# Optimization experiments

Hardware: AMD Instinct MI355X
Metric: run time of the kernel (lower is better)

## Reference

```python
import jax, jax.numpy as jnp
import numpy as np

B, S, H = 4, 2048, 1024   # batch, seq, hidden
D = 2048                  # expert intermediate (SwiGLU MLP)
E = 8                     # n_routed_experts
K = 2                     # num_experts_per_tok


def setup_inputs() -> dict:
    key = jax.random.key(0)
    ks = jax.random.split(key, 8)
    w = lambda k, shape: (jax.random.normal(k, shape, jnp.float32) * 0.02)
    return {
        "hidden_states": jax.random.normal(ks[0], (B, S, H), jnp.float32),
        "gate_w": w(ks[1], (H, E)),       # router logits projection
        "w_gate": w(ks[2], (E, H, D)),    # routed experts: gate_proj
        "w_up":   w(ks[3], (E, H, D)),    # routed experts: up_proj
        "w_down": w(ks[4], (E, D, H)),    # routed experts: down_proj
        "ws_gate": w(ks[5], (H, D)),      # shared expert: gate_proj
        "ws_up":   w(ks[6], (H, D)),      # shared expert: up_proj
        "ws_down": w(ks[7], (D, H)),      # shared expert: down_proj
    }


def reference(hidden_states, gate_w, w_gate, w_up, w_down, ws_gate, ws_up, ws_down):
    b, s, h = hidden_states.shape
    x = hidden_states.reshape(-1, h)                      # [N, H], N = B*S

    # --- MoeGate: softmax over experts, top-k, renormalize top-k weights ---
    scores = jax.nn.softmax(x @ gate_w, axis=-1)          # [N, E]
    topk_w, topk_idx = jax.lax.top_k(scores, K)           # [N, K]
    topk_w = topk_w / (jnp.sum(topk_w, axis=-1, keepdims=True) + 1e-20)

    # Combine per-token top-k weights into a dense per-expert weight [N, E].
    # Equivalent to the sort-based dispatch + index_add combine in the original:
    # each token's output is sum_k topk_w[n,k] * expert_{topk_idx[n,k]}(x[n]).
    onehot = jax.nn.one_hot(topk_idx, E, dtype=x.dtype)   # [N, K, E]
    w_per_expert = jnp.einsum('nke,nk->ne', onehot, topk_w)  # [N, E]

    # --- routed experts (SwiGLU MLP), fixed small loop over experts ---
    y = jnp.zeros_like(x)
    for e in range(E):
        hid = jax.nn.silu(x @ w_gate[e]) * (x @ w_up[e])  # [N, D]
        y = y + w_per_expert[:, e:e + 1] * (hid @ w_down[e])

    # --- shared expert applied to all tokens ---
    shared = (jax.nn.silu(x @ ws_gate) * (x @ ws_up)) @ ws_down
    return (y + shared).reshape(b, s, h)
```

## Files before the change

kernel.cpp:

```cpp
#include <hip/hip_runtime.h>
#include <hip/hip_bf16.h>
#include <stdint.h>

#define N_TOK 8192
#define H_DIM 1024
#define D_DIM 2048
#define NEXP  8

#define NSLOT      16384
#define SHARED_ROW 16512
#define HID_ROWS   24704

typedef __attribute__((ext_vector_type(8))) short          bf16x8;
typedef __attribute__((ext_vector_type(4))) float          f32x4;
typedef __attribute__((ext_vector_type(8))) unsigned short u16x8;

__device__ __forceinline__ unsigned short f2bf(float f) {
    union { float f; uint32_t u; } v; v.f = f;
    uint32_t r = v.u + 0x7fff + ((v.u >> 16) & 1);
    return (unsigned short)(r >> 16);
}

__device__ __forceinline__ void gll16(const void* g, void* l) {
    __builtin_amdgcn_global_load_lds(
        (const __attribute__((address_space(1))) void*)g,
        (__attribute__((address_space(3))) void*)l, 16, 0, 0);
}

__global__ void k_router(const float* __restrict__ x, const float* __restrict__ gw,
                         int* __restrict__ tok_e, float* __restrict__ tok_w,
                         int* __restrict__ counts) {
    int l = threadIdx.x & 63;
    int n = blockIdx.x * 4 + (threadIdx.x >> 6);
    const float* xr = x + (size_t)n * H_DIM + l * 16;
    float acc[NEXP];
#pragma unroll
    for (int e = 0; e < NEXP; ++e) acc[e] = 0.f;
#pragma unroll
    for (int j = 0; j < 16; ++j) {
        float xv = xr[j];
        const float4* g4 = (const float4*)(gw + (size_t)(l * 16 + j) * NEXP);
        float4 g0 = g4[0], g1 = g4[1];
        acc[0] += xv * g0.x; acc[1] += xv * g0.y; acc[2] += xv * g0.z; acc[3] += xv * g0.w;
        acc[4] += xv * g1.x; acc[5] += xv * g1.y; acc[6] += xv * g1.z; acc[7] += xv * g1.w;
    }
#pragma unroll
    for (int off = 32; off >= 1; off >>= 1) {
#pragma unroll
        for (int e = 0; e < NEXP; ++e) acc[e] += __shfl_xor(acc[e], off);
    }
    if (l == 0) {
        int e0 = 0; float v0 = acc[0];
#pragma unroll
        for (int e = 1; e < NEXP; ++e) if (acc[e] > v0) { v0 = acc[e]; e0 = e; }
        int e1 = -1; float v1 = -1e30f;
#pragma unroll
        for (int e = 0; e < NEXP; ++e) if (e != e0 && acc[e] > v1) { v1 = acc[e]; e1 = e; }
        float t  = expf(v1 - v0);
        float w1 = t / (1.f + t);
        float w0 = 1.f - w1;
        tok_e[2 * n]     = e0;  tok_e[2 * n + 1] = e1;
        tok_w[2 * n]     = w0;  tok_w[2 * n + 1] = w1;
        atomicAdd(&counts[e0], 1);
        atomicAdd(&counts[e1], 1);
    }
}

__global__ void k_scan(const int* __restrict__ counts, int* __restrict__ offs) {
    if (threadIdx.x == 0) {
        int s = 0;
        for (int e = 0; e < NEXP; ++e) { offs[e] = s; s += counts[e]; }
    }
}

__global__ void k_assign(const int* __restrict__ tok_e, const float* __restrict__ tok_w,
                         const int* __restrict__ offs, int* __restrict__ cursor,
                         int* __restrict__ slot_token, float* __restrict__ slot_weight) {
    int n = blockIdx.x * 256 + threadIdx.x;
#pragma unroll
    for (int k = 0; k < 2; ++k) {
        int e   = tok_e[2 * n + k];
        float w = tok_w[2 * n + k];
        int pos = atomicAdd(&cursor[e], 1);
        int s   = offs[e] + pos;
        slot_token[s]  = n;
        slot_weight[s] = w;
    }
}

__global__ void k_cvt_x(const float* __restrict__ x, unsigned short* __restrict__ xb) {
    size_t i = ((size_t)blockIdx.x * 256 + threadIdx.x) * 8;
    float4 a = *(const float4*)(x + i);
    float4 b = *(const float4*)(x + i + 4);
    u16x8 o;
    o[0] = f2bf(a.x); o[1] = f2bf(a.y); o[2] = f2bf(a.z); o[3] = f2bf(a.w);
    o[4] = f2bf(b.x); o[5] = f2bf(b.y); o[6] = f2bf(b.z); o[7] = f2bf(b.w);
    *(u16x8*)(xb + i) = o;
}

__global__ void k_tconv(const float* __restrict__ src, unsigned short* __restrict__ dst,
                        int R, int C) {
    __shared__ float tb[64][65];
    size_t mb = (size_t)blockIdx.z * (size_t)R * C;
    src += mb; dst += mb;
    int t = threadIdx.x;
    int r0 = blockIdx.y * 64, c0 = blockIdx.x * 64;
    int c4 = t & 15, rr = t >> 4;
#pragma unroll
    for (int p = 0; p < 4; ++p) {
        int r = p * 16 + rr;
        float4 v = *(const float4*)(src + (size_t)(r0 + r) * C + c0 + c4 * 4);
        tb[r][c4 * 4 + 0] = v.x; tb[r][c4 * 4 + 1] = v.y;
        tb[r][c4 * 4 + 2] = v.z; tb[r][c4 * 4 + 3] = v.w;
    }
    __syncthreads();
    int rbase = (t & 7) * 8;
#pragma unroll
    for (int p = 0; p < 2; ++p) {
        int cc = p * 32 + (t >> 3);
        u16x8 o;
#pragma unroll
        for (int j = 0; j < 8; ++j) o[j] = f2bf(tb[rbase + j][cc]);
        *(u16x8*)(dst + (size_t)(c0 + cc) * R + r0 + rbase) = o;
    }
}

__global__ __launch_bounds__(256, 4) void k_gemm1(
    const unsigned short* __restrict__ xb,
    const unsigned short* __restrict__ wg_t, const unsigned short* __restrict__ wu_t,
    const unsigned short* __restrict__ wsg_t, const unsigned short* __restrict__ wsu_t,
    const int* __restrict__ counts, const int* __restrict__ offs,
    const int* __restrict__ slot_token, const float* __restrict__ slot_weight,
    unsigned short* __restrict__ hid) {
    int g = blockIdx.z;
    int n_g, sbase, hbase;
    if (g < NEXP) { n_g = counts[g]; sbase = offs[g]; hbase = sbase; }
    else          { n_g = N_TOK;     sbase = 0;       hbase = SHARED_ROW; }
    int rt = blockIdx.y;
    if (rt * 128 >= n_g) return;
    int dt = blockIdx.x;

    const unsigned short* Bg = (g < NEXP) ? wg_t + (size_t)g * D_DIM * H_DIM : wsg_t;
    const unsigned short* Bu = (g < NEXP) ? wu_t + (size_t)g * D_DIM * H_DIM : wsu_t;

    __shared__ __attribute__((aligned(16))) char smem[32 * 1024];
    __shared__ float sWt[128];
    char* sA  = smem;
    char* sBg = smem + 16384;
    char* sBu = smem + 24576;

    int t = threadIdx.x;
    int w = t >> 6, l = t & 63;
    if (t < 128) {
        int r = rt * 128 + t;
        sWt[t] = (g < NEXP) ? ((r < n_g) ? slot_weight[sbase + r] : 0.f) : 1.f;
    }
    int lr8 = l >> 3, lc8 = l & 7;
    int swz = ((lc8 ^ lr8) << 4);

    const char* aptr[4]; char* ldsa[4];
#pragma unroll
    for (int c = 0; c < 4; ++c) {
        int chunk = w * 4 + c;
        int row = chunk * 8 + lr8;
        int r = rt * 128 + row;
        int tk;
        if (g == NEXP) tk = r;
        else           tk = (r < n_g) ? slot_token[sbase + r] : slot_token[sbase];
        aptr[c] = (const char*)xb + ((size_t)tk * H_DIM) * 2 + swz;
        ldsa[c] = sA + chunk * 1024;
    }
    const char* bgptr[2]; const char* buptr[2]; char* ldsbg[2]; char* ldsbu[2];
#pragma unroll
    for (int c = 0; c < 2; ++c) {
        int chunk = w * 2 + c;
        int row = chunk * 8 + lr8;
        int nn = dt * 64 + row;
        bgptr[c] = (const char*)Bg + ((size_t)nn * H_DIM) * 2 + swz;
        buptr[c] = (const char*)Bu + ((size_t)nn * H_DIM) * 2 + swz;
        ldsbg[c] = sBg + chunk * 1024;
        ldsbu[c] = sBu + chunk * 1024;
    }

    f32x4 accg[4][2], accu[4][2];
#pragma unroll
    for (int m = 0; m < 4; ++m)
#pragma unroll
        for (int n = 0; n < 2; ++n) { accg[m][n] = 0.f; accu[m][n] = 0.f; }

    int wr = w >> 1, wc = w & 1;
    int lr = l & 15, lg = l >> 4;
    int rsw = (lr & 7) << 4;

    for (int ks = 0; ks < H_DIM / 64; ++ks) {
        int kb = ks * 128;
#pragma unroll
        for (int c = 0; c < 4; ++c) gll16(aptr[c] + kb, ldsa[c]);
#pragma unroll
        for (int c = 0; c < 2; ++c) {
            gll16(bgptr[c] + kb, ldsbg[c]);
            gll16(buptr[c] + kb, ldsbu[c]);
        }
        __syncthreads();
#pragma unroll
        for (int ksub = 0; ksub < 2; ++ksub) {
            int c0 = (ksub * 64 + lg * 16) ^ rsw;
            bf16x8 a[4], bg[2], bu[2];
#pragma unroll
            for (int m = 0; m < 4; ++m)
                a[m] = *(const bf16x8*)(sA + (wr * 64 + m * 16 + lr) * 128 + c0);
#pragma unroll
            for (int n = 0; n < 2; ++n) {
                bg[n] = *(const bf16x8*)(sBg + (wc * 32 + n * 16 + lr) * 128 + c0);
                bu[n] = *(const bf16x8*)(sBu + (wc * 32 + n * 16 + lr) * 128 + c0);
            }
#pragma unroll
            for (int m = 0; m < 4; ++m)
#pragma unroll
                for (int n = 0; n < 2; ++n) {
                    accg[m][n] = __builtin_amdgcn_mfma_f32_16x16x32_bf16(a[m], bg[n], accg[m][n], 0, 0, 0);
                    accu[m][n] = __builtin_amdgcn_mfma_f32_16x16x32_bf16(a[m], bu[n], accu[m][n], 0, 0, 0);
                }
        }
        __syncthreads();
    }

    int cb = dt * 64 + wc * 32;
#pragma unroll
    for (int m = 0; m < 4; ++m)
#pragma unroll
        for (int n = 0; n < 2; ++n)
#pragma unroll
            for (int i = 0; i < 4; ++i) {
                int trow = wr * 64 + m * 16 + lg * 4 + i;
                int row = rt * 128 + trow;
                if (row < n_g) {
                    float gv = accg[m][n][i], uv = accu[m][n][i];
                    float hv = (gv / (1.f + __expf(-gv))) * uv * sWt[trow];
                    int col = cb + n * 16 + lr;
                    hid[(size_t)(hbase + row) * D_DIM + col] = f2bf(hv);
                }
            }
}

template <int MODE>
__global__ __launch_bounds__(256, 4) void k_gemm2(
    const unsigned short* __restrict__ hid,
    const unsigned short* __restrict__ wd_t, const unsigned short* __restrict__ wsd_t,
    const int* __restrict__ counts, const int* __restrict__ offs,
    const int* __restrict__ slot_token, float* __restrict__ out) {
    int n_g, abase;
    const unsigned short* B;
    if (MODE == 0) { n_g = N_TOK; abase = SHARED_ROW; B = wsd_t; }
    else {
        int g = blockIdx.z;
        n_g = counts[g]; abase = offs[g];
        B = wd_t + (size_t)g * H_DIM * D_DIM;
    }
    int rt = blockIdx.y;
    if (rt * 128 >= n_g) return;
    int ct = blockIdx.x;

    __shared__ __attribute__((aligned(16))) char smem[24 * 1024];
    __shared__ int sTok[128];
    char* sA = smem;
    char* sB = smem + 16384;

    int t = threadIdx.x, w = t >> 6, l = t & 63;
    if (MODE == 1 && t < 128) {
        int r = rt * 128 + t;
        sTok[t] = (r < n_g) ? slot_token[abase + r] : 0;
    }
    int lr8 = l >> 3, lc8 = l & 7;
    int swz = ((lc8 ^ lr8) << 4);
    const char* aptr[4]; char* ldsa[4];
#pragma unroll
    for (int c = 0; c < 4; ++c) {
        int chunk = w * 4 + c;
        int row = chunk * 8 + lr8;
        aptr[c] = (const char*)hid + ((size_t)(abase + rt * 128 + row) * D_DIM) * 2 + swz;
        ldsa[c] = sA + chunk * 1024;
    }
    const char* bptr[2]; char* ldsb[2];
#pragma unroll
    for (int c = 0; c < 2; ++c) {
        int chunk = w * 2 + c;
        int row = chunk * 8 + lr8;
        bptr[c] = (const char*)B + ((size_t)(ct * 64 + row) * D_DIM) * 2 + swz;
        ldsb[c] = sB + chunk * 1024;
    }
    f32x4 acc[4][2];
#pragma unroll
    for (int m = 0; m < 4; ++m)
#pragma unroll
        for (int n = 0; n < 2; ++n) acc[m][n] = 0.f;

    int wr = w >> 1, wc = w & 1, lr = l & 15, lg = l >> 4;
    int rsw = (lr & 7) << 4;

    for (int ks = 0; ks < D_DIM / 64; ++ks) {
        int kb = ks * 128;
#pragma unroll
        for (int c = 0; c < 4; ++c) gll16(aptr[c] + kb, ldsa[c]);
#pragma unroll
        for (int c = 0; c < 2; ++c) gll16(bptr[c] + kb, ldsb[c]);
        __syncthreads();
#pragma unroll
        for (int ksub = 0; ksub < 2; ++ksub) {
            int c0 = (ksub * 64 + lg * 16) ^ rsw;
            bf16x8 a[4], b[2];
#pragma unroll
            for (int m = 0; m < 4; ++m)
                a[m] = *(const bf16x8*)(sA + (wr * 64 + m * 16 + lr) * 128 + c0);
#pragma unroll
            for (int n = 0; n < 2; ++n)
                b[n] = *(const bf16x8*)(sB + (wc * 32 + n * 16 + lr) * 128 + c0);
#pragma unroll
            for (int m = 0; m < 4; ++m)
#pragma unroll
                for (int n = 0; n < 2; ++n)
                    acc[m][n] = __builtin_amdgcn_mfma_f32_16x16x32_bf16(a[m], b[n], acc[m][n], 0, 0, 0);
        }
        __syncthreads();
    }

    int cb = ct * 64 + wc * 32;
#pragma unroll
    for (int m = 0; m < 4; ++m)
#pragma unroll
        for (int n = 0; n < 2; ++n)
#pragma unroll
            for (int i = 0; i < 4; ++i) {
                int tr = wr * 64 + m * 16 + lg * 4 + i;
                int col = cb + n * 16 + lr;
                if (MODE == 0) {
                    out[(size_t)(rt * 128 + tr) * H_DIM + col] = acc[m][n][i];
                } else {
                    if (rt * 128 + tr < n_g) {
                        int tok = sTok[tr];
                        unsafeAtomicAdd(&out[(size_t)tok * H_DIM + col], acc[m][n][i]);
                    }
                }
            }
}

extern "C" void kernel_launch(void* const* d_in, const int* in_sizes, int n_in,
                              void* d_out, int out_size, void* d_ws, size_t ws_size,
                              hipStream_t stream) {
    const float* x       = (const float*)d_in[0];
    const float* gw      = (const float*)d_in[1];
    const float* w_gate  = (const float*)d_in[2];
    const float* w_up    = (const float*)d_in[3];
    const float* w_down  = (const float*)d_in[4];
    const float* ws_gate = (const float*)d_in[5];
    const float* ws_up   = (const float*)d_in[6];
    const float* ws_down = (const float*)d_in[7];
    float* out = (float*)d_out;
    char* ws = (char*)d_ws;

    const size_t oXB    = 0;
    const size_t oWG    = oXB    + (size_t)N_TOK * H_DIM * 2;
    const size_t oWU    = oWG    + (size_t)NEXP * D_DIM * H_DIM * 2;
    const size_t oWD    = oWU    + (size_t)NEXP * D_DIM * H_DIM * 2;
    const size_t oWSG   = oWD    + (size_t)NEXP * H_DIM * D_DIM * 2;
    const size_t oWSU   = oWSG   + (size_t)D_DIM * H_DIM * 2;
    const size_t oWSD   = oWSU   + (size_t)D_DIM * H_DIM * 2;
    const size_t oHID   = oWSD   + (size_t)H_DIM * D_DIM * 2;
    const size_t oTOKE  = oHID   + (size_t)HID_ROWS * D_DIM * 2;
    const size_t oTOKW  = oTOKE  + (size_t)N_TOK * 2 * 4;
    const size_t oSLOTT = oTOKW  + (size_t)N_TOK * 2 * 4;
    const size_t oSLOTW = oSLOTT + (size_t)(NSLOT + 128) * 4;
    const size_t oCTRL  = oSLOTW + (size_t)(NSLOT + 128) * 4;

    unsigned short* xb    = (unsigned short*)(ws + oXB);
    unsigned short* wg_t  = (unsigned short*)(ws + oWG);
    unsigned short* wu_t  = (unsigned short*)(ws + oWU);
    unsigned short* wd_t  = (unsigned short*)(ws + oWD);
    unsigned short* wsg_t = (unsigned short*)(ws + oWSG);
    unsigned short* wsu_t = (unsigned short*)(ws + oWSU);
    unsigned short* wsd_t = (unsigned short*)(ws + oWSD);
    unsigned short* hid   = (unsigned short*)(ws + oHID);
    int*   tok_e       = (int*)(ws + oTOKE);
    float* tok_w       = (float*)(ws + oTOKW);
    int*   slot_token  = (int*)(ws + oSLOTT);
    float* slot_weight = (float*)(ws + oSLOTW);
    int*   counts      = (int*)(ws + oCTRL);
    int*   offs        = counts + 8;
    int*   cursor      = counts + 16;

    hipMemsetAsync(counts, 0, 256, stream);
    k_router<<<N_TOK / 4, 256, 0, stream>>>(x, gw, tok_e, tok_w, counts);
    k_scan<<<1, 64, 0, stream>>>(counts, offs);
    k_assign<<<N_TOK / 256, 256, 0, stream>>>(tok_e, tok_w, offs, cursor, slot_token, slot_weight);

    k_cvt_x<<<(N_TOK * H_DIM) / (8 * 256), 256, 0, stream>>>(x, xb);
    k_tconv<<<dim3(D_DIM / 64, H_DIM / 64, NEXP), 256, 0, stream>>>(w_gate, wg_t, H_DIM, D_DIM);
    k_tconv<<<dim3(D_DIM / 64, H_DIM / 64, NEXP), 256, 0, stream>>>(w_up,   wu_t, H_DIM, D_DIM);
    k_tconv<<<dim3(H_DIM / 64, D_DIM / 64, NEXP), 256, 0, stream>>>(w_down, wd_t, D_DIM, H_DIM);
    k_tconv<<<dim3(D_DIM / 64, H_DIM / 64, 1),    256, 0, stream>>>(ws_gate, wsg_t, H_DIM, D_DIM);
    k_tconv<<<dim3(D_DIM / 64, H_DIM / 64, 1),    256, 0, stream>>>(ws_up,   wsu_t, H_DIM, D_DIM);
    k_tconv<<<dim3(H_DIM / 64, D_DIM / 64, 1),    256, 0, stream>>>(ws_down, wsd_t, D_DIM, H_DIM);

    k_gemm1<<<dim3(32, 64, NEXP + 1), 256, 0, stream>>>(xb, wg_t, wu_t, wsg_t, wsu_t,
                                                        counts, offs, slot_token, slot_weight, hid);
    k_gemm2<0><<<dim3(16, 64, 1), 256, 0, stream>>>(hid, wd_t, wsd_t, counts, offs,
                                                    slot_token, out);
    k_gemm2<1><<<dim3(16, 64, NEXP), 256, 0, stream>>>(hid, wd_t, wsd_t, counts, offs,
                                                       slot_token, out);
}
```

Measured before the change: 936.4 us.

## Fuse routing/dispatch, merge weight conversions, replace atomic combine with slot buffer

```diff
diff --git a/kernel.cpp b/kernel.cpp
--- a/kernel.cpp
+++ b/kernel.cpp
@@ -29,82 +29,112 @@
 
 __global__ void k_router(const float* __restrict__ x, const float* __restrict__ gw,
                          int* __restrict__ tok_e, float* __restrict__ tok_w,
-                         int* __restrict__ counts) {
+                         unsigned short* __restrict__ xb) {
     int l = threadIdx.x & 63;
     int n = blockIdx.x * 4 + (threadIdx.x >> 6);
-    const float* xr = x + (size_t)n * H_DIM + l * 16;
+    const float4* xr4 = (const float4*)(x + (size_t)n * H_DIM + l * 16);
+    float4 v0 = xr4[0], v1 = xr4[1], v2 = xr4[2], v3 = xr4[3];
+    float xv[16] = {v0.x, v0.y, v0.z, v0.w, v1.x, v1.y, v1.z, v1.w,
+                    v2.x, v2.y, v2.z, v2.w, v3.x, v3.y, v3.z, v3.w};
     float acc[NEXP];
 #pragma unroll
     for (int e = 0; e < NEXP; ++e) acc[e] = 0.f;
 #pragma unroll
     for (int j = 0; j < 16; ++j) {
-        float xv = xr[j];
+        float xvj = xv[j];
         const float4* g4 = (const float4*)(gw + (size_t)(l * 16 + j) * NEXP);
         float4 g0 = g4[0], g1 = g4[1];
-        acc[0] += xv * g0.x; acc[1] += xv * g0.y; acc[2] += xv * g0.z; acc[3] += xv * g0.w;
-        acc[4] += xv * g1.x; acc[5] += xv * g1.y; acc[6] += xv * g1.z; acc[7] += xv * g1.w;
-    }
+        acc[0] += xvj * g0.x; acc[1] += xvj * g0.y; acc[2] += xvj * g0.z; acc[3] += xvj * g0.w;
+        acc[4] += xvj * g1.x; acc[5] += xvj * g1.y; acc[6] += xvj * g1.z; acc[7] += xvj * g1.w;
+    }
+    u16x8 o0, o1;
+#pragma unroll
+    for (int j = 0; j < 8; ++j) { o0[j] = f2bf(xv[j]); o1[j] = f2bf(xv[j + 8]); }
+    unsigned short* xbr = xb + (size_t)n * H_DIM + l * 16;
+    *(u16x8*)(xbr)     = o0;
+    *(u16x8*)(xbr + 8) = o1;
+
 #pragma unroll
     for (int off = 32; off >= 1; off >>= 1) {
 #pragma unroll
         for (int e = 0; e < NEXP; ++e) acc[e] += __shfl_xor(acc[e], off);
     }
     if (l == 0) {
-        int e0 = 0; float v0 = acc[0];
-#pragma unroll
-        for (int e = 1; e < NEXP; ++e) if (acc[e] > v0) { v0 = acc[e]; e0 = e; }
-        int e1 = -1; float v1 = -1e30f;
-#pragma unroll
-        for (int e = 0; e < NEXP; ++e) if (e != e0 && acc[e] > v1) { v1 = acc[e]; e1 = e; }
-        float t  = expf(v1 - v0);
+        int e0 = 0; float v0m = acc[0];
+#pragma unroll
+        for (int e = 1; e < NEXP; ++e) if (acc[e] > v0m) { v0m = acc[e]; e0 = e; }
+        int e1 = -1; float v1m = -1e30f;
+#pragma unroll
+        for (int e = 0; e < NEXP; ++e) if (e != e0 && acc[e] > v1m) { v1m = acc[e]; e1 = e; }
+        float t  = expf(v1m - v0m);
         float w1 = t / (1.f + t);
         float w0 = 1.f - w1;
         tok_e[2 * n]     = e0;  tok_e[2 * n + 1] = e1;
         tok_w[2 * n]     = w0;  tok_w[2 * n + 1] = w1;
-        atomicAdd(&counts[e0], 1);
-        atomicAdd(&counts[e1], 1);
-    }
-}
-
-__global__ void k_scan(const int* __restrict__ counts, int* __restrict__ offs) {
-    if (threadIdx.x == 0) {
-        int s = 0;
-        for (int e = 0; e < NEXP; ++e) { offs[e] = s; s += counts[e]; }
-    }
-}
-
-__global__ void k_assign(const int* __restrict__ tok_e, const float* __restrict__ tok_w,
-                         const int* __restrict__ offs, int* __restrict__ cursor,
-                         int* __restrict__ slot_token, float* __restrict__ slot_weight) {
-    int n = blockIdx.x * 256 + threadIdx.x;
-#pragma unroll
-    for (int k = 0; k < 2; ++k) {
-        int e   = tok_e[2 * n + k];
-        float w = tok_w[2 * n + k];
-        int pos = atomicAdd(&cursor[e], 1);
-        int s   = offs[e] + pos;
-        slot_token[s]  = n;
-        slot_weight[s] = w;
-    }
-}
-
-__global__ void k_cvt_x(const float* __restrict__ x, unsigned short* __restrict__ xb) {
-    size_t i = ((size_t)blockIdx.x * 256 + threadIdx.x) * 8;
-    float4 a = *(const float4*)(x + i);
-    float4 b = *(const float4*)(x + i + 4);
-    u16x8 o;
-    o[0] = f2bf(a.x); o[1] = f2bf(a.y); o[2] = f2bf(a.z); o[3] = f2bf(a.w);
-    o[4] = f2bf(b.x); o[5] = f2bf(b.y); o[6] = f2bf(b.z); o[7] = f2bf(b.w);
-    *(u16x8*)(xb + i) = o;
-}
-
-__global__ void k_tconv(const float* __restrict__ src, unsigned short* __restrict__ dst,
-                        int R, int C) {
+    }
+}
+
+__global__ __launch_bounds__(512) void k_dispatch(
+    const int* __restrict__ tok_e, const float* __restrict__ tok_w,
+    int* __restrict__ counts, int* __restrict__ offs,
+    int* __restrict__ slot_token, float* __restrict__ slot_weight,
+    int* __restrict__ slot_of) {
+    __shared__ int se[2 * N_TOK];
+    __shared__ int scnt[NEXP];
+    int t = threadIdx.x, w = t >> 6, l = t & 63;
+    for (int i = t; i < 2 * N_TOK; i += 512) se[i] = tok_e[i];
+    __syncthreads();
+    int cnt = 0;
+    for (int i = l; i < 2 * N_TOK; i += 64) cnt += (se[i] == w) ? 1 : 0;
+#pragma unroll
+    for (int off = 32; off >= 1; off >>= 1) cnt += __shfl_xor(cnt, off);
+    if (l == 0) scnt[w] = cnt;
+    __syncthreads();
+    if (t < NEXP) {
+        int b = 0;
+        for (int e = 0; e < t; ++e) b += scnt[e];
+        offs[t]   = b;
+        counts[t] = scnt[t];
+    }
+    int run = 0;
+    for (int e = 0; e < w; ++e) run += scnt[e];
+    for (int i0 = 0; i0 < 2 * N_TOK; i0 += 64) {
+        int i = i0 + l;
+        bool mine = (se[i] == w);
+        unsigned long long m = __ballot(mine);
+        int pos = __popcll(m & ((1ull << l) - 1ull));
+        if (mine) {
+            int s = run + pos;
+            slot_token[s]  = i >> 1;
+            slot_weight[s] = tok_w[i];
+            slot_of[i]     = s;
+        }
+        run += __popcll(m);
+    }
+}
+
+__global__ void k_tconv_all(const float* __restrict__ w_gate, const float* __restrict__ w_up,
+                            const float* __restrict__ w_down,
+                            const float* __restrict__ ws_gate, const float* __restrict__ ws_up,
+                            const float* __restrict__ ws_down,
+                            unsigned short* __restrict__ wg_t, unsigned short* __restrict__ wu_t,
+                            unsigned short* __restrict__ wd_t,
+                            unsigned short* __restrict__ wsg_t, unsigned short* __restrict__ wsu_t,
+                            unsigned short* __restrict__ wsd_t) {
     __shared__ float tb[64][65];
-    size_t mb = (size_t)blockIdx.z * (size_t)R * C;
-    src += mb; dst += mb;
+    int z = blockIdx.y;
+    const float* src; unsigned short* dst; int R, C;
+    if (z < 8)       { R = H_DIM; C = D_DIM; src = w_gate + (size_t)z * R * C;        dst = wg_t + (size_t)z * R * C; }
+    else if (z < 16) { R = H_DIM; C = D_DIM; src = w_up   + (size_t)(z - 8) * R * C;  dst = wu_t + (size_t)(z - 8) * R * C; }
+    else if (z < 24) { R = D_DIM; C = H_DIM; src = w_down + (size_t)(z - 16) * R * C; dst = wd_t + (size_t)(z - 16) * R * C; }
+    else if (z == 24){ R = H_DIM; C = D_DIM; src = ws_gate; dst = wsg_t; }
+    else if (z == 25){ R = H_DIM; C = D_DIM; src = ws_up;   dst = wsu_t; }
+    else             { R = D_DIM; C = H_DIM; src = ws_down; dst = wsd_t; }
+    int ncx = C >> 6;
+    int bx = blockIdx.x;
+    int c0 = (bx % ncx) * 64, r0 = (bx / ncx) * 64;
+
     int t = threadIdx.x;
-    int r0 = blockIdx.y * 64, c0 = blockIdx.x * 64;
     int c4 = t & 15, rr = t >> 4;
 #pragma unroll
     for (int p = 0; p < 4; ++p) {
@@ -248,7 +278,7 @@
     const unsigned short* __restrict__ hid,
     const unsigned short* __restrict__ wd_t, const unsigned short* __restrict__ wsd_t,
     const int* __restrict__ counts, const int* __restrict__ offs,
-    const int* __restrict__ slot_token, float* __restrict__ out) {
+    float* __restrict__ y_slot, float* __restrict__ out) {
     int n_g, abase;
     const unsigned short* B;
     if (MODE == 0) { n_g = N_TOK; abase = SHARED_ROW; B = wsd_t; }
@@ -262,15 +292,10 @@
     int ct = blockIdx.x;
 
     __shared__ __attribute__((aligned(16))) char smem[24 * 1024];
-    __shared__ int sTok[128];
     char* sA = smem;
     char* sB = smem + 16384;
 
     int t = threadIdx.x, w = t >> 6, l = t & 63;
-    if (MODE == 1 && t < 128) {
-        int r = rt * 128 + t;
-        sTok[t] = (r < n_g) ? slot_token[abase + r] : 0;
-    }
     int lr8 = l >> 3, lc8 = l & 7;
     int swz = ((lc8 ^ lr8) << 4);
     const char* aptr[4]; char* ldsa[4];
@@ -336,12 +361,23 @@
                 if (MODE == 0) {
                     out[(size_t)(rt * 128 + tr) * H_DIM + col] = acc[m][n][i];
                 } else {
-                    if (rt * 128 + tr < n_g) {
-                        int tok = sTok[tr];
-                        unsafeAtomicAdd(&out[(size_t)tok * H_DIM + col], acc[m][n][i]);
-                    }
+                    int row = rt * 128 + tr;
+                    if (row < n_g)
+                        y_slot[(size_t)(abase + row) * H_DIM + col] = acc[m][n][i];
                 }
             }
+}
+
+__global__ void k_combine(const float* __restrict__ y_slot, const int* __restrict__ slot_of,
+                          float* __restrict__ out) {
+    int n = blockIdx.x * 2 + (threadIdx.x >> 7);
+    int c = (threadIdx.x & 127) * 8;
+    int s0 = slot_of[2 * n], s1 = slot_of[2 * n + 1];
+    const f32x4* p0 = (const f32x4*)(y_slot + (size_t)s0 * H_DIM + c);
+    const f32x4* p1 = (const f32x4*)(y_slot + (size_t)s1 * H_DIM + c);
+    f32x4* po = (f32x4*)(out + (size_t)n * H_DIM + c);
+    po[0] += p0[0] + p1[0];
+    po[1] += p0[1] + p1[1];
 }
 
 extern "C" void kernel_launch(void* const* d_in, const int* in_sizes, int n_in,
@@ -370,7 +406,8 @@
     const size_t oTOKW  = oTOKE  + (size_t)N_TOK * 2 * 4;
     const size_t oSLOTT = oTOKW  + (size_t)N_TOK * 2 * 4;
     const size_t oSLOTW = oSLOTT + (size_t)(NSLOT + 128) * 4;
-    const size_t oCTRL  = oSLOTW + (size_t)(NSLOT + 128) * 4;
+    const size_t oSLOTO = oSLOTW + (size_t)(NSLOT + 128) * 4;
+    const size_t oCTRL  = oSLOTO + (size_t)N_TOK * 2 * 4;
 
     unsigned short* xb    = (unsigned short*)(ws + oXB);
     unsigned short* wg_t  = (unsigned short*)(ws + oWG);
@@ -380,31 +417,26 @@
     unsigned short* wsu_t = (unsigned short*)(ws + oWSU);
     unsigned short* wsd_t = (unsigned short*)(ws + oWSD);
     unsigned short* hid   = (unsigned short*)(ws + oHID);
+    float* y_slot      = (float*)(ws + oWG);
     int*   tok_e       = (int*)(ws + oTOKE);
     float* tok_w       = (float*)(ws + oTOKW);
     int*   slot_token  = (int*)(ws + oSLOTT);
     float* slot_weight = (float*)(ws + oSLOTW);
+    int*   slot_of     = (int*)(ws + oSLOTO);
     int*   counts      = (int*)(ws + oCTRL);
     int*   offs        = counts + 8;
-    int*   cursor      = counts + 16;
-
-    hipMemsetAsync(counts, 0, 256, stream);
-    k_router<<<N_TOK / 4, 256, 0, stream>>>(x, gw, tok_e, tok_w, counts);
-    k_scan<<<1, 64, 0, stream>>>(counts, offs);
-    k_assign<<<N_TOK / 256, 256, 0, stream>>>(tok_e, tok_w, offs, cursor, slot_token, slot_weight);
-
-    k_cvt_x<<<(N_TOK * H_DIM) / (8 * 256), 256, 0, stream>>>(x, xb);
-    k_tconv<<<dim3(D_DIM / 64, H_DIM / 64, NEXP), 256, 0, stream>>>(w_gate, wg_t, H_DIM, D_DIM);
-    k_tconv<<<dim3(D_DIM / 64, H_DIM / 64, NEXP), 256, 0, stream>>>(w_up,   wu_t, H_DIM, D_DIM);
-    k_tconv<<<dim3(H_DIM / 64, D_DIM / 64, NEXP), 256, 0, stream>>>(w_down, wd_t, D_DIM, H_DIM);
-    k_tconv<<<dim3(D_DIM / 64, H_DIM / 64, 1),    256, 0, stream>>>(ws_gate, wsg_t, H_DIM, D_DIM);
-    k_tconv<<<dim3(D_DIM / 64, H_DIM / 64, 1),    256, 0, stream>>>(ws_up,   wsu_t, H_DIM, D_DIM);
-    k_tconv<<<dim3(H_DIM / 64, D_DIM / 64, 1),    256, 0, stream>>>(ws_down, wsd_t, D_DIM, H_DIM);
-
+
+    k_router<<<N_TOK / 4, 256, 0, stream>>>(x, gw, tok_e, tok_w, xb);
+    k_dispatch<<<1, 512, 0, stream>>>(tok_e, tok_w, counts, offs,
+                                      slot_token, slot_weight, slot_of);
+    k_tconv_all<<<dim3(512, 27), 256, 0, stream>>>(w_gate, w_up, w_down,
+                                                   ws_gate, ws_up, ws_down,
+                                                   wg_t, wu_t, wd_t, wsg_t, wsu_t, wsd_t);
     k_gemm1<<<dim3(32, 64, NEXP + 1), 256, 0, stream>>>(xb, wg_t, wu_t, wsg_t, wsu_t,
                                                         counts, offs, slot_token, slot_weight, hid);
+    k_gemm2<1><<<dim3(16, 64, NEXP), 256, 0, stream>>>(hid, wd_t, wsd_t, counts, offs,
+                                                       y_slot, out);
     k_gemm2<0><<<dim3(16, 64, 1), 256, 0, stream>>>(hid, wd_t, wsd_t, counts, offs,
-                                                    slot_token, out);
-    k_gemm2<1><<<dim3(16, 64, NEXP), 256, 0, stream>>>(hid, wd_t, wsd_t, counts, offs,
-                                                       slot_token, out);
-}
+                                                    y_slot, out);
+    k_combine<<<N_TOK / 2, 256, 0, stream>>>(y_slot, slot_of, out);
+}
```

Measured after the change: 759.3 us. -18.9%, faster.
